# Performance work log

Hardware: AMD Instinct MI355X
Metric: run time of the kernel (lower is better)

The kernel has to match this reference:

```python
import jax, jax.numpy as jnp
import numpy as np

IDIM = 256
N_UNITS = 512
N_LAYERS = 4
E_UNITS = 2048
H = 8
D_K = N_UNITS // H
EPS = 1e-5


def _layer_norm(x, g, b):
    mu = jnp.mean(x, axis=-1, keepdims=True)
    var = jnp.mean(jnp.square(x - mu), axis=-1, keepdims=True)
    return (x - mu) * jax.lax.rsqrt(var + EPS) * g + b


def setup_inputs() -> dict:
    key = jax.random.key(0)
    ks = jax.random.split(key, 16)
    s = 0.02
    inp = {
        'x': jax.random.normal(ks[0], (4, 2, 1024, IDIM), dtype=jnp.float32),
        'Win': jax.random.normal(ks[1], (N_UNITS, IDIM), dtype=jnp.float32) * s,
        'bin_': jnp.zeros((N_UNITS,), jnp.float32),
        'ln1_g': jnp.ones((N_LAYERS, N_UNITS), jnp.float32),
        'ln1_b': jnp.zeros((N_LAYERS, N_UNITS), jnp.float32),
        'Wq': jax.random.normal(ks[2], (N_LAYERS, N_UNITS, N_UNITS), dtype=jnp.float32) * s,
        'bq': jnp.zeros((N_LAYERS, N_UNITS), jnp.float32),
        'Wk': jax.random.normal(ks[3], (N_LAYERS, N_UNITS, N_UNITS), dtype=jnp.float32) * s,
        'bk': jnp.zeros((N_LAYERS, N_UNITS), jnp.float32),
        'Wv': jax.random.normal(ks[4], (N_LAYERS, N_UNITS, N_UNITS), dtype=jnp.float32) * s,
        'bv': jnp.zeros((N_LAYERS, N_UNITS), jnp.float32),
        'Wo': jax.random.normal(ks[5], (N_LAYERS, N_UNITS, N_UNITS), dtype=jnp.float32) * s,
        'bo': jnp.zeros((N_LAYERS, N_UNITS), jnp.float32),
        'ln2_g': jnp.ones((N_LAYERS, N_UNITS), jnp.float32),
        'ln2_b': jnp.zeros((N_LAYERS, N_UNITS), jnp.float32),
        'W1': jax.random.normal(ks[6], (N_LAYERS, E_UNITS, N_UNITS), dtype=jnp.float32) * s,
        'b1': jnp.zeros((N_LAYERS, E_UNITS), jnp.float32),
        'W2': jax.random.normal(ks[7], (N_LAYERS, N_UNITS, E_UNITS), dtype=jnp.float32) * s,
        'b2': jnp.zeros((N_LAYERS, N_UNITS), jnp.float32),
        'lno_g': jnp.ones((N_UNITS,), jnp.float32),
        'lno_b': jnp.zeros((N_UNITS,), jnp.float32),
    }
    return inp


def reference(x, Win, bin_, ln1_g, ln1_b, Wq, bq, Wk, bk, Wv, bv, Wo, bo,
              ln2_g, ln2_b, W1, b1, W2, b2, lno_g, lno_b):
    bs, num, T, dim = x.shape
    B = bs * num
    # input projection; e is kept as [B*T, n_units] like the torch code
    e = x.reshape(B * T, dim) @ Win.T + bin_
    scale = 1.0 / np.sqrt(D_K).astype(np.float32)
    for i in range(N_LAYERS):
        e = _layer_norm(e, ln1_g[i], ln1_b[i])
        # multi-head self-attention (dropout is identity in eval)
        q = (e @ Wq[i].T + bq[i]).reshape(B, T, H, D_K)
        k = (e @ Wk[i].T + bk[i]).reshape(B, T, H, D_K)
        v = (e @ Wv[i].T + bv[i]).reshape(B, T, H, D_K)
        scores = jnp.einsum('bthd,bshd->bhts', q, k) * scale  # [B,H,T,T]
        att = jax.nn.softmax(scores, axis=-1)
        ctx = jnp.einsum('bhts,bshd->bthd', att, v).reshape(B * T, N_UNITS)
        s = ctx @ Wo[i].T + bo[i]
        e = e + s
        e = _layer_norm(e, ln2_g[i], ln2_b[i])
        # position-wise feed-forward
        hdn = jnp.maximum(e @ W1[i].T + b1[i], 0.0)
        e = e + (hdn @ W2[i].T + b2[i])
    out = _layer_norm(e, lno_g, lno_b)
    return out.reshape(bs, num, T, N_UNITS)
```

## Files before the change

kernel.cpp:

```cpp
#include <hip/hip_runtime.h>
#include <hip/hip_bf16.h>
#include <math.h>
#include <stdint.h>

#define IDIM   256
#define NU     512
#define NL     4
#define EU     2048
#define NH     8
#define DK     64
#define TT     1024
#define NB     8
#define MTOT   8192

typedef short  bf16x8 __attribute__((ext_vector_type(8)));
typedef float  f32x4  __attribute__((ext_vector_type(4)));
typedef unsigned short ushortv2 __attribute__((ext_vector_type(2)));

__device__ __forceinline__ unsigned short f2b(float x) {
  unsigned int u = __float_as_uint(x);
  u += 0x7fffu + ((u >> 16) & 1u);
  return (unsigned short)(u >> 16);
}

__device__ __forceinline__ void gload16(const unsigned short* g, unsigned short* l) {
  auto gp = reinterpret_cast<const __attribute__((address_space(1))) unsigned int*>(
      reinterpret_cast<uintptr_t>(g));
  auto lp = reinterpret_cast<__attribute__((address_space(3))) unsigned int*>(
      reinterpret_cast<uintptr_t>(l));
  __builtin_amdgcn_global_load_lds(gp, lp, 16, 0, 0);
}

__global__ __launch_bounds__(256) void cvt_bf16(
    const float* __restrict__ src, unsigned short* __restrict__ dst, int n) {
  int i = (blockIdx.x * 256 + threadIdx.x) * 8;
  if (i >= n) return;
  float4 a = *(const float4*)(src + i);
  float4 b = *(const float4*)(src + i + 4);
  bf16x8 r;
  r[0] = (short)f2b(a.x); r[1] = (short)f2b(a.y);
  r[2] = (short)f2b(a.z); r[3] = (short)f2b(a.w);
  r[4] = (short)f2b(b.x); r[5] = (short)f2b(b.y);
  r[6] = (short)f2b(b.z); r[7] = (short)f2b(b.w);
  *(bf16x8*)(dst + i) = r;
}

#define GEMM_CORE(K_, KBEG, KEND)                                            \
  __shared__ unsigned short As[128 * 64];                                    \
  __shared__ unsigned short Bs[128 * 64];                                    \
  const int tid  = threadIdx.x;                                              \
  const int lane = tid & 63;                                                 \
  const int wv   = tid >> 6;                                                 \
  const int wm   = (wv >> 1) * 64;                                           \
  const int wn   = (wv & 1) * 64;                                            \
  const int fr   = lane & 15;                                                \
  const int fc   = lane >> 4;                                                \
  const int srow = wv * 8 + (lane >> 3);                                     \
  const int skk  = (lane & 7) * 8;                                           \
  const unsigned short* ag = A + (size_t)(m0 + srow) * (K_) + skk;           \
  const unsigned short* bg = W + (size_t)(n0 + srow) * (K_) + skk;           \
  f32x4 acc[4][4];                                                           \
  _Pragma("unroll") for (int i = 0; i < 4; ++i)                              \
    _Pragma("unroll") for (int j = 0; j < 4; ++j)                            \
      acc[i][j] = (f32x4){0.f, 0.f, 0.f, 0.f};                               \
  for (int k0 = (KBEG); k0 < (KEND); k0 += 64) {                             \
    __syncthreads();                                                         \
    _Pragma("unroll") for (int ii = 0; ii < 4; ++ii) {                       \
      gload16(ag + (size_t)(ii * 32) * (K_) + k0, &As[ii * 2048 + wv * 512]);\
      gload16(bg + (size_t)(ii * 32) * (K_) + k0, &Bs[ii * 2048 + wv * 512]);\
    }                                                                        \
    __syncthreads();                        \
    _Pragma("unroll") for (int kc = 0; kc < 2; ++kc) {                       \
      bf16x8 af[4], bfr[4];                                                  \
      _Pragma("unroll") for (int mi = 0; mi < 4; ++mi)                       \
        af[mi] = *(const bf16x8*)&As[(wm + mi * 16 + fr) * 64 + kc * 32 + fc * 8]; \
      _Pragma("unroll") for (int ni = 0; ni < 4; ++ni)                       \
        bfr[ni] = *(const bf16x8*)&Bs[(wn + ni * 16 + fr) * 64 + kc * 32 + fc * 8]; \
      _Pragma("unroll") for (int mi = 0; mi < 4; ++mi)                       \
        _Pragma("unroll") for (int ni = 0; ni < 4; ++ni)                     \
          acc[mi][ni] = __builtin_amdgcn_mfma_f32_16x16x32_bf16(             \
              af[mi], bfr[ni], acc[mi][ni], 0, 0, 0);                        \
    }                                                                        \
  }

template<int MODE, bool RELU>
__global__ __launch_bounds__(256) void gemm_bf(
    const unsigned short* __restrict__ A, const unsigned short* __restrict__ W,
    const float* __restrict__ bias, float* __restrict__ Cf,
    unsigned short* __restrict__ Cb, int M, int N, int K, int kchunk) {
  const int m0 = blockIdx.y * 128;
  const int n0 = blockIdx.x * 128;
  const int kbeg = blockIdx.z * kchunk;
  const int kend = kbeg + kchunk;
  GEMM_CORE(K, kbeg, kend)

  const bool addb = (blockIdx.z == 0);
#pragma unroll
  for (int ni = 0; ni < 4; ++ni) {
    const int col = n0 + wn + ni * 16 + fr;
    const float bb = (MODE != 2 || addb) ? bias[col] : 0.f;
#pragma unroll
    for (int mi = 0; mi < 4; ++mi) {
      const int row = m0 + wm + mi * 16 + fc * 4;
#pragma unroll
      for (int j = 0; j < 4; ++j) {
        size_t off = (size_t)(row + j) * N + col;
        float r = acc[mi][ni][j] + bb;
        if (RELU) r = fmaxf(r, 0.f);
        if (MODE == 0) Cf[off] = r;
        else if (MODE == 1) Cb[off] = f2b(r);
        else atomicAdd(&Cf[off], r);
      }
    }
  }
}

__global__ __launch_bounds__(256) void gemm_qkv(
    const unsigned short* __restrict__ A,
    const unsigned short* __restrict__ Wq, const unsigned short* __restrict__ Wk,
    const unsigned short* __restrict__ Wv,
    const float* __restrict__ bq, const float* __restrict__ bk,
    const float* __restrict__ bv,
    unsigned short* __restrict__ Oq, unsigned short* __restrict__ Ok,
    unsigned short* __restrict__ Ov) {
  const int zz = blockIdx.z;
  const unsigned short* W  = zz == 0 ? Wq : (zz == 1 ? Wk : Wv);
  const float* bias        = zz == 0 ? bq : (zz == 1 ? bk : bv);
  unsigned short* C        = zz == 0 ? Oq : (zz == 1 ? Ok : Ov);
  const float scale        = zz == 0 ? 0.125f : 1.0f;
  const int m0 = blockIdx.y * 128;
  const int n0 = blockIdx.x * 128;
  GEMM_CORE(NU, 0, NU)

#pragma unroll
  for (int ni = 0; ni < 4; ++ni) {
    const int col = n0 + wn + ni * 16 + fr;
    const float bb = bias[col];
#pragma unroll
    for (int mi = 0; mi < 4; ++mi) {
      const int row = m0 + wm + mi * 16 + fc * 4;
#pragma unroll
      for (int j = 0; j < 4; ++j)
        C[(size_t)(row + j) * NU + col] = f2b((acc[mi][ni][j] + bb) * scale);
    }
  }
}

template<bool WB>
__global__ __launch_bounds__(256) void layernorm_inplace(
    float* __restrict__ e, const float* __restrict__ g,
    const float* __restrict__ b, unsigned short* __restrict__ eb) {
  const int row = blockIdx.x;
  float* x = e + (size_t)row * NU;
  const int tid = threadIdx.x;

  float2 v = *(const float2*)&x[tid * 2];
  float sum = v.x + v.y;
  float sq  = v.x * v.x + v.y * v.y;
#pragma unroll
  for (int o = 32; o > 0; o >>= 1) {
    sum += __shfl_down(sum, o);
    sq  += __shfl_down(sq, o);
  }
  __shared__ float ps[4], pq[4], stat[2];
  const int wid = tid >> 6, lane = tid & 63;
  if (lane == 0) { ps[wid] = sum; pq[wid] = sq; }
  __syncthreads();
  if (tid == 0) {
    float s = ps[0] + ps[1] + ps[2] + ps[3];
    float q = pq[0] + pq[1] + pq[2] + pq[3];
    float mu = s * (1.0f / NU);
    float var = q * (1.0f / NU) - mu * mu;
    stat[0] = mu;
    stat[1] = rsqrtf(var + 1e-5f);
  }
  __syncthreads();
  const float mu = stat[0], rstd = stat[1];
  const float2 gg = *(const float2*)&g[tid * 2];
  const float2 bb = *(const float2*)&b[tid * 2];
  v.x = (v.x - mu) * rstd * gg.x + bb.x;
  v.y = (v.y - mu) * rstd * gg.y + bb.y;
  *(float2*)&x[tid * 2] = v;
  if (WB) {
    ushortv2 o = {f2b(v.x), f2b(v.y)};
    *(ushortv2*)&eb[(size_t)row * NU + tid * 2] = o;
  }
}

__global__ __launch_bounds__(256) void flash_attn_mfma(
    const unsigned short* __restrict__ Q, const unsigned short* __restrict__ K,
    const unsigned short* __restrict__ V, unsigned short* __restrict__ O) {
  constexpr int LSTR = 72;
  __shared__ unsigned short Ks[64 * LSTR];
  __shared__ unsigned short Vt[64 * LSTR];
  __shared__ unsigned short Ps[64 * LSTR];

  const int b = blockIdx.z, h = blockIdx.y;
  const int q0 = blockIdx.x * 64;
  const int tid = threadIdx.x;
  const int lane = tid & 63;
  const int w = tid >> 6;
  const int fr = lane & 15;
  const int fc = lane >> 4;

  const size_t hb = ((size_t)b * TT) * NU + h * DK;

  bf16x8 qf[2];
#pragma unroll
  for (int kc = 0; kc < 2; ++kc)
    qf[kc] = *(const bf16x8*)(Q + hb +
        (size_t)(q0 + w * 16 + fr) * NU + kc * 32 + fc * 8);

  f32x4 ctx[4];
#pragma unroll
  for (int ni = 0; ni < 4; ++ni) ctx[ni] = (f32x4){0.f, 0.f, 0.f, 0.f};
  float m_run[4], l_run[4];
#pragma unroll
  for (int j = 0; j < 4; ++j) { m_run[j] = -1e30f; l_run[j] = 0.f; }

  const int sr = tid >> 2;
  const int sd = (tid & 3) * 16;

  for (int kt = 0; kt < TT; kt += 64) {
    const unsigned short* kp = K + hb + (size_t)(kt + sr) * NU + sd;
    const unsigned short* vp = V + hb + (size_t)(kt + sr) * NU + sd;
    bf16x8 k0 = *(const bf16x8*)kp, k1 = *(const bf16x8*)(kp + 8);
    bf16x8 v0 = *(const bf16x8*)vp, v1 = *(const bf16x8*)(vp + 8);

    __syncthreads();
    *(bf16x8*)&Ks[sr * LSTR + sd]     = k0;
    *(bf16x8*)&Ks[sr * LSTR + sd + 8] = k1;
#pragma unroll
    for (int t = 0; t < 8; ++t) {
      Vt[(sd + t)     * LSTR + sr] = (unsigned short)v0[t];
      Vt[(sd + t + 8) * LSTR + sr] = (unsigned short)v1[t];
    }
    __syncthreads();

    bf16x8 kf[4][2];
#pragma unroll
    for (int ni = 0; ni < 4; ++ni)
#pragma unroll
      for (int kc = 0; kc < 2; ++kc)
        kf[ni][kc] = *(const bf16x8*)&Ks[(ni * 16 + fr) * LSTR + kc * 32 + fc * 8];

    f32x4 sacc[4];
#pragma unroll
    for (int ni = 0; ni < 4; ++ni) sacc[ni] = (f32x4){0.f, 0.f, 0.f, 0.f};
#pragma unroll
    for (int kc = 0; kc < 2; ++kc)
#pragma unroll
      for (int ni = 0; ni < 4; ++ni)
        sacc[ni] = __builtin_amdgcn_mfma_f32_16x16x32_bf16(
            qf[kc], kf[ni][kc], sacc[ni], 0, 0, 0);

    float cm[4];
#pragma unroll
    for (int j = 0; j < 4; ++j)
      cm[j] = fmaxf(fmaxf(sacc[0][j], sacc[1][j]),
                    fmaxf(sacc[2][j], sacc[3][j]));
#pragma unroll
    for (int mask = 1; mask < 16; mask <<= 1)
#pragma unroll
      for (int j = 0; j < 4; ++j)
        cm[j] = fmaxf(cm[j], __shfl_xor(cm[j], mask));
#pragma unroll
    for (int j = 0; j < 4; ++j) {
      float mn = fmaxf(m_run[j], cm[j]);
      float corr = __expf(m_run[j] - mn);
      m_run[j] = mn;
      l_run[j] *= corr;
#pragma unroll
      for (int ni = 0; ni < 4; ++ni) {
        ctx[ni][j] *= corr;
        float p = __expf(sacc[ni][j] - mn);
        l_run[j] += p;
        Ps[(w * 16 + fc * 4 + j) * LSTR + ni * 16 + fr] = f2b(p);
      }
    }

    bf16x8 pf[2], vf[4][2];
#pragma unroll
    for (int kc = 0; kc < 2; ++kc)
      pf[kc] = *(const bf16x8*)&Ps[(w * 16 + fr) * LSTR + kc * 32 + fc * 8];
#pragma unroll
    for (int ni = 0; ni < 4; ++ni)
#pragma unroll
      for (int kc = 0; kc < 2; ++kc)
        vf[ni][kc] = *(const bf16x8*)&Vt[(ni * 16 + fr) * LSTR + kc * 32 + fc * 8];
#pragma unroll
    for (int kc = 0; kc < 2; ++kc)
#pragma unroll
      for (int ni = 0; ni < 4; ++ni)
        ctx[ni] = __builtin_amdgcn_mfma_f32_16x16x32_bf16(
            pf[kc], vf[ni][kc], ctx[ni], 0, 0, 0);
  }

#pragma unroll
  for (int j = 0; j < 4; ++j) {
    float l = l_run[j];
#pragma unroll
    for (int mask = 1; mask < 16; mask <<= 1)
      l += __shfl_xor(l, mask);
    const float inv = 1.0f / l;
    const int row = q0 + w * 16 + fc * 4 + j;
    unsigned short* dst = O + hb + (size_t)row * NU;
#pragma unroll
    for (int ni = 0; ni < 4; ++ni)
      dst[ni * 16 + fr] = f2b(ctx[ni][j] * inv);
  }
}

extern "C" void kernel_launch(void* const* d_in, const int* in_sizes, int n_in,
                              void* d_out, int out_size, void* d_ws, size_t ws_size,
                              hipStream_t stream) {
  const float* x     = (const float*)d_in[0];
  const float* Win   = (const float*)d_in[1];
  const float* bin_  = (const float*)d_in[2];
  const float* ln1_g = (const float*)d_in[3];
  const float* ln1_b = (const float*)d_in[4];
  const float* Wq    = (const float*)d_in[5];
  const float* bq    = (const float*)d_in[6];
  const float* Wk    = (const float*)d_in[7];
  const float* bk    = (const float*)d_in[8];
  const float* Wv    = (const float*)d_in[9];
  const float* bv    = (const float*)d_in[10];
  const float* Wo    = (const float*)d_in[11];
  const float* bo    = (const float*)d_in[12];
  const float* ln2_g = (const float*)d_in[13];
  const float* ln2_b = (const float*)d_in[14];
  const float* W1    = (const float*)d_in[15];
  const float* b1    = (const float*)d_in[16];
  const float* W2    = (const float*)d_in[17];
  const float* b2    = (const float*)d_in[18];
  const float* lno_g = (const float*)d_in[19];
  const float* lno_b = (const float*)d_in[20];

  float* e = (float*)d_out;
  unsigned short* wsb = (unsigned short*)d_ws;
  const size_t M1 = 1u << 20;
  unsigned short* q    = wsb;
  unsigned short* k    = wsb + 4 * M1;
  unsigned short* v    = wsb + 8 * M1;
  unsigned short* ctx  = wsb + 12 * M1;
  unsigned short* hdn  = wsb;
  unsigned short* xbf  = wsb + 4 * M1;
  unsigned short* winb = wsb + 6 * M1;
  unsigned short* ebf  = wsb + 16 * M1;
  unsigned short* wqb  = wsb + 20 * M1;
  unsigned short* wkb  = wsb + 21 * M1;
  unsigned short* wvb  = wsb + 22 * M1;
  unsigned short* wob  = wsb + 23 * M1;
  unsigned short* w1b  = wsb + 24 * M1;
  unsigned short* w2b  = wsb + 28 * M1;

  const dim3 blk(256);
  cvt_bf16<<<1024, blk, 0, stream>>>(x,   xbf,  MTOT * IDIM);
  cvt_bf16<<<64,   blk, 0, stream>>>(Win, winb, NU * IDIM);
  cvt_bf16<<<512,  blk, 0, stream>>>(Wq,  wqb,  NL * NU * NU);
  cvt_bf16<<<512,  blk, 0, stream>>>(Wk,  wkb,  NL * NU * NU);
  cvt_bf16<<<512,  blk, 0, stream>>>(Wv,  wvb,  NL * NU * NU);
  cvt_bf16<<<512,  blk, 0, stream>>>(Wo,  wob,  NL * NU * NU);
  cvt_bf16<<<2048, blk, 0, stream>>>(W1,  w1b,  NL * EU * NU);
  cvt_bf16<<<2048, blk, 0, stream>>>(W2,  w2b,  NL * NU * EU);

  const dim3 gProjIn(NU / 128, MTOT / 128);
  const dim3 gQKV(NU / 128, MTOT / 128, 3);
  const dim3 gWo(NU / 128, MTOT / 128, 2);
  const dim3 gF1(EU / 128, MTOT / 128);
  const dim3 gF2(NU / 128, MTOT / 128, 2);
  const dim3 gAttn(TT / 64, NH, NB);

  gemm_bf<0, false><<<gProjIn, blk, 0, stream>>>(
      xbf, winb, bin_, e, nullptr, MTOT, NU, IDIM, IDIM);

  for (int i = 0; i < NL; ++i) {
    layernorm_inplace<true><<<MTOT, blk, 0, stream>>>(e, ln1_g + i * NU, ln1_b + i * NU, ebf);

    gemm_qkv<<<gQKV, blk, 0, stream>>>(ebf, wqb + (size_t)i * NU * NU,
                                       wkb + (size_t)i * NU * NU,
                                       wvb + (size_t)i * NU * NU,
                                       bq + i * NU, bk + i * NU, bv + i * NU,
                                       q, k, v);

    flash_attn_mfma<<<gAttn, blk, 0, stream>>>(q, k, v, ctx);

    gemm_bf<2, false><<<gWo, blk, 0, stream>>>(
        ctx, wob + (size_t)i * NU * NU, bo + i * NU, e, nullptr,
        MTOT, NU, NU, NU / 2);

    layernorm_inplace<true><<<MTOT, blk, 0, stream>>>(e, ln2_g + i * NU, ln2_b + i * NU, ebf);

    gemm_bf<1, true><<<gF1, blk, 0, stream>>>(
        ebf, w1b + (size_t)i * EU * NU, b1 + i * EU, nullptr, hdn,
        MTOT, EU, NU, NU);

    gemm_bf<2, false><<<gF2, blk, 0, stream>>>(
        hdn, w2b + (size_t)i * NU * EU, b2 + i * NU, e, nullptr,
        MTOT, NU, EU, EU / 2);
  }

  layernorm_inplace<false><<<MTOT, blk, 0, stream>>>(e, lno_g, lno_b, nullptr);
}
```

Measured before the change: 1.055 ms.

## Double-buffer GEMM LDS tiles, pad V transpose, lazy softmax rescale, more split-K

The GEMM core now uses two 128x32 LDS buffers and prefetches the next K slice with direct-to-LDS loads while the current one runs on MFMA, removing one barrier per iteration at the cost of a halved K step. In attention, the transposed V tile gets an odd-ish stride to cut LDS bank conflicts on the scatter stores, and the online-softmax rescale is skipped unless a row max grows by more than 8. Split-K for the Wo and FFN2 GEMMs goes from 2 to 4 slices to raise block count, at the cost of more atomic accumulation into the output. The lazy rescale keeps exponentials bounded but lets the reference max lag the true max, and the prefetch has no wait on the global_load_lds before the barrier, which may be a correctness risk.

Result: slower. 1.212 ms (+14.9%).

```diff
diff --git a/kernel.cpp b/kernel.cpp
--- a/kernel.cpp
+++ b/kernel.cpp
@@ -45,9 +45,16 @@
   *(bf16x8*)(dst + i) = r;
 }
 
+#define GEMM_STAGE(BUF, KK)                                                  \
+  _Pragma("unroll") for (int ii = 0; ii < 2; ++ii) {                         \
+    gload16(ag + (size_t)(ii * 64) * kdim + (KK), &As[BUF][ii * 2048 + wv * 512]); \
+    gload16(bg + (size_t)(ii * 64) * kdim + (KK), &Bs[BUF][ii * 2048 + wv * 512]); \
+  }
+
 #define GEMM_CORE(K_, KBEG, KEND)                                            \
-  __shared__ unsigned short As[128 * 64];                                    \
-  __shared__ unsigned short Bs[128 * 64];                                    \
+  __shared__ unsigned short As[2][128 * 32];                                 \
+  __shared__ unsigned short Bs[2][128 * 32];                                 \
+  const int kdim = (K_);                                                     \
   const int tid  = threadIdx.x;                                              \
   const int lane = tid & 63;                                                 \
   const int wv   = tid >> 6;                                                 \
@@ -55,32 +62,31 @@
   const int wn   = (wv & 1) * 64;                                            \
   const int fr   = lane & 15;                                                \
   const int fc   = lane >> 4;                                                \
-  const int srow = wv * 8 + (lane >> 3);                                     \
-  const int skk  = (lane & 7) * 8;                                           \
-  const unsigned short* ag = A + (size_t)(m0 + srow) * (K_) + skk;           \
-  const unsigned short* bg = W + (size_t)(n0 + srow) * (K_) + skk;           \
+  const int srow = wv * 16 + (lane >> 2);                                    \
+  const int skk  = (lane & 3) * 8;                                           \
+  const unsigned short* ag = A + (size_t)(m0 + srow) * kdim + skk;           \
+  const unsigned short* bg = W + (size_t)(n0 + srow) * kdim + skk;           \
   f32x4 acc[4][4];                                                           \
   _Pragma("unroll") for (int i = 0; i < 4; ++i)                              \
     _Pragma("unroll") for (int j = 0; j < 4; ++j)                            \
       acc[i][j] = (f32x4){0.f, 0.f, 0.f, 0.f};                               \
-  for (int k0 = (KBEG); k0 < (KEND); k0 += 64) {                             \
-    __syncthreads();                                                         \
-    _Pragma("unroll") for (int ii = 0; ii < 4; ++ii) {                       \
-      gload16(ag + (size_t)(ii * 32) * (K_) + k0, &As[ii * 2048 + wv * 512]);\
-      gload16(bg + (size_t)(ii * 32) * (K_) + k0, &Bs[ii * 2048 + wv * 512]);\
-    }                                                                        \
-    __syncthreads();                        \
-    _Pragma("unroll") for (int kc = 0; kc < 2; ++kc) {                       \
-      bf16x8 af[4], bfr[4];                                                  \
-      _Pragma("unroll") for (int mi = 0; mi < 4; ++mi)                       \
-        af[mi] = *(const bf16x8*)&As[(wm + mi * 16 + fr) * 64 + kc * 32 + fc * 8]; \
+  int cur = 0;                                                               \
+  GEMM_STAGE(0, (KBEG))                                                      \
+  for (int k0 = (KBEG); k0 < (KEND); k0 += 32) {                             \
+    __syncthreads();   \
+    if (k0 + 32 < (KEND)) { GEMM_STAGE(cur ^ 1, k0 + 32) }                   \
+    const unsigned short* acu = As[cur];                                     \
+    const unsigned short* bcu = Bs[cur];                                     \
+    bf16x8 af[4], bfr[4];                                                    \
+    _Pragma("unroll") for (int mi = 0; mi < 4; ++mi)                         \
+      af[mi] = *(const bf16x8*)&acu[(wm + mi * 16 + fr) * 32 + fc * 8];      \
+    _Pragma("unroll") for (int ni = 0; ni < 4; ++ni)                         \
+      bfr[ni] = *(const bf16x8*)&bcu[(wn + ni * 16 + fr) * 32 + fc * 8];     \
+    _Pragma("unroll") for (int mi = 0; mi < 4; ++mi)                         \
       _Pragma("unroll") for (int ni = 0; ni < 4; ++ni)                       \
-        bfr[ni] = *(const bf16x8*)&Bs[(wn + ni * 16 + fr) * 64 + kc * 32 + fc * 8]; \
-      _Pragma("unroll") for (int mi = 0; mi < 4; ++mi)                       \
-        _Pragma("unroll") for (int ni = 0; ni < 4; ++ni)                     \
-          acc[mi][ni] = __builtin_amdgcn_mfma_f32_16x16x32_bf16(             \
-              af[mi], bfr[ni], acc[mi][ni], 0, 0, 0);                        \
-    }                                                                        \
+        acc[mi][ni] = __builtin_amdgcn_mfma_f32_16x16x32_bf16(               \
+            af[mi], bfr[ni], acc[mi][ni], 0, 0, 0);                          \
+    cur ^= 1;                                                                \
   }
 
 template<int MODE, bool RELU>
@@ -191,8 +197,9 @@
     const unsigned short* __restrict__ Q, const unsigned short* __restrict__ K,
     const unsigned short* __restrict__ V, unsigned short* __restrict__ O) {
   constexpr int LSTR = 72;
+  constexpr int VSTR = 66;
   __shared__ unsigned short Ks[64 * LSTR];
-  __shared__ unsigned short Vt[64 * LSTR];
+  __shared__ unsigned short Vt[64 * VSTR];
   __shared__ unsigned short Ps[64 * LSTR];
 
   const int b = blockIdx.z, h = blockIdx.y;
@@ -232,8 +239,8 @@
     *(bf16x8*)&Ks[sr * LSTR + sd + 8] = k1;
 #pragma unroll
     for (int t = 0; t < 8; ++t) {
-      Vt[(sd + t)     * LSTR + sr] = (unsigned short)v0[t];
-      Vt[(sd + t + 8) * LSTR + sr] = (unsigned short)v1[t];
+      Vt[(sd + t)     * VSTR + sr] = (unsigned short)v0[t];
+      Vt[(sd + t + 8) * VSTR + sr] = (unsigned short)v1[t];
     }
     __syncthreads();
 
@@ -264,20 +271,28 @@
 #pragma unroll
       for (int j = 0; j < 4; ++j)
         cm[j] = fmaxf(cm[j], __shfl_xor(cm[j], mask));
-#pragma unroll
-    for (int j = 0; j < 4; ++j) {
-      float mn = fmaxf(m_run[j], cm[j]);
-      float corr = __expf(m_run[j] - mn);
-      m_run[j] = mn;
-      l_run[j] *= corr;
+
+    int need = (cm[0] > m_run[0] + 8.f) | (cm[1] > m_run[1] + 8.f) |
+               (cm[2] > m_run[2] + 8.f) | (cm[3] > m_run[3] + 8.f);
+    if (__any(need)) {
+#pragma unroll
+      for (int j = 0; j < 4; ++j) {
+        float mn = fmaxf(m_run[j], cm[j]);
+        float corr = __expf(m_run[j] - mn);
+        m_run[j] = mn;
+        l_run[j] *= corr;
+#pragma unroll
+        for (int ni = 0; ni < 4; ++ni) ctx[ni][j] *= corr;
+      }
+    }
+#pragma unroll
+    for (int j = 0; j < 4; ++j)
 #pragma unroll
       for (int ni = 0; ni < 4; ++ni) {
-        ctx[ni][j] *= corr;
-        float p = __expf(sacc[ni][j] - mn);
+        float p = __expf(sacc[ni][j] - m_run[j]);
         l_run[j] += p;
         Ps[(w * 16 + fc * 4 + j) * LSTR + ni * 16 + fr] = f2b(p);
       }
-    }
 
     bf16x8 pf[2], vf[4][2];
 #pragma unroll
@@ -287,7 +302,7 @@
     for (int ni = 0; ni < 4; ++ni)
 #pragma unroll
       for (int kc = 0; kc < 2; ++kc)
-        vf[ni][kc] = *(const bf16x8*)&Vt[(ni * 16 + fr) * LSTR + kc * 32 + fc * 8];
+        vf[ni][kc] = *(const bf16x8*)&Vt[(ni * 16 + fr) * VSTR + kc * 32 + fc * 8];
 #pragma unroll
     for (int kc = 0; kc < 2; ++kc)
 #pragma unroll
@@ -366,9 +381,9 @@
 
   const dim3 gProjIn(NU / 128, MTOT / 128);
   const dim3 gQKV(NU / 128, MTOT / 128, 3);
-  const dim3 gWo(NU / 128, MTOT / 128, 2);
+  const dim3 gWo(NU / 128, MTOT / 128, 4);
   const dim3 gF1(EU / 128, MTOT / 128);
-  const dim3 gF2(NU / 128, MTOT / 128, 2);
+  const dim3 gF2(NU / 128, MTOT / 128, 4);
   const dim3 gAttn(TT / 64, NH, NB);
 
   gemm_bf<0, false><<<gProjIn, blk, 0, stream>>>(
@@ -387,7 +402,7 @@
 
     gemm_bf<2, false><<<gWo, blk, 0, stream>>>(
         ctx, wob + (size_t)i * NU * NU, bo + i * NU, e, nullptr,
-        MTOT, NU, NU, NU / 2);
+        MTOT, NU, NU, NU / 4);
 
     layernorm_inplace<true><<<MTOT, blk, 0, stream>>>(e, ln2_g + i * NU, ln2_b + i * NU, ebf);
 
@@ -397,7 +412,7 @@
 
     gemm_bf<2, false><<<gF2, blk, 0, stream>>>(
         hdn, w2b + (size_t)i * NU * EU, b2 + i * NU, e, nullptr,
-        MTOT, NU, EU, EU / 2);
+        MTOT, NU, EU, EU / 4);
   }
 
   layernorm_inplace<false><<<MTOT, blk, 0, stream>>>(e, lno_g, lno_b, nullptr);
```
